# Performance work log

Hardware: AMD Instinct MI355X
Metric: run time of the kernel (lower is better)

## Reference

```python
import jax, jax.numpy as jnp
import numpy as np


def _mlp(h, W_in, b_in, W_hid, b_hid, W_out, b_out):
    # 392 -> 1000 -> (1000)x4 -> 392, ReLU between linear layers (NICE shift net)
    h = jax.nn.relu(h @ W_in + b_in)
    for i in range(W_hid.shape[0]):  # fixed small layer count, not a data dim
        h = jax.nn.relu(h @ W_hid[i] + b_hid[i])
    return h @ W_out + b_out


def setup_inputs() -> dict:
    key = jax.random.key(0)
    ks = jax.random.split(key, 4)
    B, D, MID = 4096, 784, 1000
    half = D // 2
    return {
        "x": jax.random.normal(ks[0], (B, D), jnp.float32),
        "log_det_J": jnp.zeros((1,), jnp.float32),
        "W_in": jax.random.normal(ks[1], (half, MID), jnp.float32) * 0.05,
        "b_in": jnp.zeros((MID,), jnp.float32),
        "W_hid": jax.random.normal(ks[2], (4, MID, MID), jnp.float32) * 0.03,
        "b_hid": jnp.zeros((4, MID), jnp.float32),
        "W_out": jax.random.normal(ks[3], (MID, half), jnp.float32) * 0.03,
        "b_out": jnp.zeros((half,), jnp.float32),
    }


def reference(x, log_det_J, W_in, b_in, W_hid, b_hid, W_out, b_out):
    # mask_config = 0: first = even columns, second = odd columns
    first = x[:, 0::2]   # (B, D/2)
    second = x[:, 1::2]  # (B, D/2)
    shift = _mlp(first, W_in, b_in, W_hid, b_hid, W_out, b_out)
    y_second = second + shift  # coupling_law (reverse=False)
    # interleave: y[:, 0::2] = first, y[:, 1::2] = y_second, in one strided write
    y = jnp.stack([first, y_second], axis=2).reshape(x.shape)
    return (y, log_det_J)
```

## Files before the change

### kernel.cpp

```cpp
#include <hip/hip_runtime.h>

typedef __bf16 bf16;
typedef __bf16 bf16x8 __attribute__((ext_vector_type(8)));
typedef float f32x4 __attribute__((ext_vector_type(4)));

#define M_TOT 4096
#define D_IN  784
#define HALF  392
#define MID   1000
#define K0PAD 448
#define NPAD  1024

__device__ __forceinline__ void g2l16(const bf16* g, bf16* l) {
  __builtin_amdgcn_global_load_lds(
      (__attribute__((address_space(1))) void*)(g),
      (__attribute__((address_space(3))) void*)(l),
      16, 0, 0);
}

__device__ __forceinline__ void wtrans_tile(const float* __restrict__ W, bf16* __restrict__ WT,
                                            int K, int N, int Kpad, int tn, int tk,
                                            float (*tb)[33], int tid) {
  int n0 = tn * 32, k0 = tk * 32;
  int tx = tid & 31, ty = tid >> 5;
#pragma unroll
  for (int r = 0; r < 4; ++r) {
    int k = k0 + ty + 8 * r, n = n0 + tx;
    tb[ty + 8 * r][tx] = (k < K && n < N) ? W[(size_t)k * N + n] : 0.f;
  }
  __syncthreads();
#pragma unroll
  for (int r = 0; r < 4; ++r) {
    int n = n0 + ty + 8 * r, k = k0 + tx;
    WT[(size_t)n * Kpad + k] = (bf16)tb[tx][ty + 8 * r];
  }
}

__global__ void prep_k(const float* __restrict__ x, const float* __restrict__ ldj,
                       const float* __restrict__ W_in,
                       bf16* __restrict__ A0, bf16* __restrict__ WT0,
                       float* __restrict__ y) {
  __shared__ float tb[32][33];
  const int b = blockIdx.x, tid = threadIdx.x;
  if (b < 896) {
    int g = b * 256 + tid;
    int m = g / 56;
    int kq = g - m * 56, k0 = kq * 8;
    bf16x8 v;
    if (k0 < HALF) {
      const float4* xr = (const float4*)(x + (size_t)m * D_IN + 2 * k0);
      float4 a0 = xr[0], a1 = xr[1], a2 = xr[2], a3 = xr[3];
      v[0] = (bf16)a0.x; v[1] = (bf16)a0.z;
      v[2] = (bf16)a1.x; v[3] = (bf16)a1.z;
      v[4] = (bf16)a2.x; v[5] = (bf16)a2.z;
      v[6] = (bf16)a3.x; v[7] = (bf16)a3.z;
    } else {
#pragma unroll
      for (int j = 0; j < 8; ++j) v[j] = (bf16)0.f;
    }
    *(bf16x8*)(A0 + (size_t)m * K0PAD + k0) = v;
    if (b == 0 && tid == 0) y[(size_t)M_TOT * D_IN] = ldj[0];
    return;
  }
  int u = b - 896;
  wtrans_tile(W_in, WT0, HALF, MID, K0PAD, u & 31, u >> 5, tb, tid);
}

template <int BM, int BN, int EPI, int K>
__global__ __launch_bounds__(256, (BM > 64 ? 2 : 4))
void gemm_k(const bf16* __restrict__ A, const bf16* __restrict__ BT,
            const float* __restrict__ bias, int bias_n,
            bf16* __restrict__ C,
            const float* __restrict__ x, float* __restrict__ y, int nb,
            const float* __restrict__ Wx, bf16* __restrict__ WTx,
            int wK, int wN, int wKpad, int wTN) {
  constexpr int BK = 64;
  constexpr int MT = BM / 32, NT = BN / 32;
  constexpr int KT = K / BK;
  constexpr int NBM = M_TOT / BM;
  alignas(16) __shared__ bf16 ldsA[BM * BK];
  alignas(16) __shared__ bf16 ldsB[BN * BK];
  const int tid = threadIdx.x;
  const int id = blockIdx.x;

  if (id >= nb) {
    int u = id - nb;
    wtrans_tile(Wx, WTx, wK, wN, wKpad, u % wTN, u / wTN, (float(*)[33])ldsA, tid);
    return;
  }

  const int wave = tid >> 6, lane = tid & 63;
  const int bm = id % NBM, bn = id / NBM;

  const int srow = lane >> 3;
  const int sq = (lane & 7) ^ srow;
  const bf16* gA = A + ((size_t)bm * BM + wave * (BM / 4) + srow) * K + sq * 8;
  const bf16* gB = BT + ((size_t)bn * BN + wave * (BN / 4) + srow) * K + sq * 8;
  bf16* lA = &ldsA[wave * (BM / 4) * BK];
  bf16* lB = &ldsB[wave * (BN / 4) * BK];

  const int mlane = lane & 15, quad = lane >> 4;
  const int wm = (wave & 1) * (BM / 2), wn = (wave >> 1) * (BN / 2);
  const int axor = mlane & 7;
  const bf16* raBase = &ldsA[(wm + mlane) * BK];
  const bf16* rbBase = &ldsB[(wn + mlane) * BK];

  f32x4 acc[MT][NT] = {};

#pragma unroll
  for (int i = 0; i < BM / 32; ++i) g2l16(gA + (size_t)(8 * i) * K, lA + (8 * i) * BK);
#pragma unroll
  for (int i = 0; i < BN / 32; ++i) g2l16(gB + (size_t)(8 * i) * K, lB + (8 * i) * BK);

  for (int kt = 0; kt < KT; ++kt) {
    __syncthreads();
    bf16x8 af[2][MT], bfr[2][NT];
#pragma unroll
    for (int s = 0; s < 2; ++s) {
      const int co = ((s * 4 + quad) ^ axor) * 8;
#pragma unroll
      for (int i = 0; i < MT; ++i) af[s][i] = *(const bf16x8*)(raBase + i * 16 * BK + co);
#pragma unroll
      for (int i = 0; i < NT; ++i) bfr[s][i] = *(const bf16x8*)(rbBase + i * 16 * BK + co);
    }
    __syncthreads();
    if (kt + 1 < KT) {
      const size_t off = (size_t)(kt + 1) * BK;
#pragma unroll
      for (int i = 0; i < BM / 32; ++i) g2l16(gA + off + (size_t)(8 * i) * K, lA + (8 * i) * BK);
#pragma unroll
      for (int i = 0; i < BN / 32; ++i) g2l16(gB + off + (size_t)(8 * i) * K, lB + (8 * i) * BK);
    }
#pragma unroll
    for (int s = 0; s < 2; ++s)
#pragma unroll
      for (int mt = 0; mt < MT; ++mt)
#pragma unroll
        for (int nt = 0; nt < NT; ++nt)
          acc[mt][nt] = __builtin_amdgcn_mfma_f32_16x16x32_bf16(
              af[s][mt], bfr[s][nt], acc[mt][nt], 0, 0, 0);
  }

  const int ng0 = bn * BN + wn + mlane;
  const int mg0 = bm * BM + wm + quad * 4;

  if (EPI == 0) {
    float bv[NT];
#pragma unroll
    for (int nt = 0; nt < NT; ++nt) {
      int n = ng0 + nt * 16;
      bv[nt] = (n < bias_n) ? bias[n] : 0.f;
    }
#pragma unroll
    for (int mt = 0; mt < MT; ++mt)
#pragma unroll
      for (int nt = 0; nt < NT; ++nt)
#pragma unroll
        for (int r = 0; r < 4; ++r) {
          int m = mg0 + mt * 16 + r;
          int n = ng0 + nt * 16;
          float v = fmaxf(acc[mt][nt][r] + bv[nt], 0.f);
          C[(size_t)m * NPAD + n] = (bf16)v;
        }
  } else {
    const float2* x2 = (const float2*)x;
    float2* y2 = (float2*)y;
#pragma unroll
    for (int nt = 0; nt < NT; ++nt) {
      int n = ng0 + nt * 16;
      if (n < HALF) {
        float bb = bias[n];
#pragma unroll
        for (int mt = 0; mt < MT; ++mt)
#pragma unroll
          for (int r = 0; r < 4; ++r) {
            int m = mg0 + mt * 16 + r;
            size_t off = (size_t)m * (D_IN / 2) + n;
            float2 v = x2[off];
            v.y += acc[mt][nt][r] + bb;
            y2[off] = v;
          }
      }
    }
  }
}

extern "C" void kernel_launch(void* const* d_in, const int* in_sizes, int n_in,
                              void* d_out, int out_size, void* d_ws, size_t ws_size,
                              hipStream_t stream) {
  const float* x     = (const float*)d_in[0];
  const float* ldj   = (const float*)d_in[1];
  const float* W_in  = (const float*)d_in[2];
  const float* b_in  = (const float*)d_in[3];
  const float* W_hid = (const float*)d_in[4];
  const float* b_hid = (const float*)d_in[5];
  const float* W_out = (const float*)d_in[6];
  const float* b_out = (const float*)d_in[7];
  float* y = (float*)d_out;

  char* p = (char*)d_ws;
  bf16* A0  = (bf16*)(p + 0);
  bf16* H0  = (bf16*)(p + 3670016);
  bf16* H1  = (bf16*)(p + 12058624);
  bf16* WT0 = (bf16*)(p + 20447232);
  bf16* WTh = (bf16*)(p + 21364736);
  bf16* WT5 = (bf16*)(p + 29753344);

  const size_t WH = (size_t)NPAD * NPAD;
  const size_t WS = (size_t)MID * MID;

  prep_k<<<dim3(896 + 448), 256, 0, stream>>>(x, ldj, W_in, A0, WT0, y);

  gemm_k<128, 64, 0, K0PAD><<<dim3(512 + 1024), 256, 0, stream>>>(
      A0, WT0, b_in, MID, H0, nullptr, nullptr, 512,
      W_hid + 0 * WS, WTh + 0 * WH, MID, MID, NPAD, 32);
  gemm_k<128, 64, 0, NPAD><<<dim3(512 + 1024), 256, 0, stream>>>(
      H0, WTh + 0 * WH, b_hid + 0 * MID, MID, H1, nullptr, nullptr, 512,
      W_hid + 1 * WS, WTh + 1 * WH, MID, MID, NPAD, 32);
  gemm_k<128, 64, 0, NPAD><<<dim3(512 + 1024), 256, 0, stream>>>(
      H1, WTh + 1 * WH, b_hid + 1 * MID, MID, H0, nullptr, nullptr, 512,
      W_hid + 2 * WS, WTh + 2 * WH, MID, MID, NPAD, 32);
  gemm_k<128, 64, 0, NPAD><<<dim3(512 + 1024), 256, 0, stream>>>(
      H0, WTh + 2 * WH, b_hid + 2 * MID, MID, H1, nullptr, nullptr, 512,
      W_hid + 3 * WS, WTh + 3 * WH, MID, MID, NPAD, 32);
  gemm_k<128, 64, 0, NPAD><<<dim3(512 + 512), 256, 0, stream>>>(
      H1, WTh + 3 * WH, b_hid + 3 * MID, MID, H0, nullptr, nullptr, 512,
      W_out, WT5, MID, HALF, NPAD, 16);
  gemm_k<64, 64, 1, NPAD><<<dim3(512), 256, 0, stream>>>(
      H0, WT5, b_out, HALF, nullptr, x, y, 512,
      nullptr, nullptr, 0, 0, 0, 1);
}
```

Before: 173.4 us.

## Double-buffer LDS tiles with two-stage prefetch and explicit vmcnt waits

Gives the GEMM two LDS buffers for each operand and prefetches two k-tiles ahead. The loop waits with s_waitcnt vmcnt on only the older stage instead of draining every load at a full __syncthreads. This keeps global-to-LDS loads in flight while MFMA runs, to hide memory latency. LDS use doubles, and launch bounds are fixed at 2 waves per EU for all tile sizes, which may lower occupancy for the 64x64 output kernel.

```diff
diff --git a/kernel.cpp b/kernel.cpp
--- a/kernel.cpp
+++ b/kernel.cpp
@@ -67,7 +67,7 @@
 }
 
 template <int BM, int BN, int EPI, int K>
-__global__ __launch_bounds__(256, (BM > 64 ? 2 : 4))
+__global__ __launch_bounds__(256, 2)
 void gemm_k(const bf16* __restrict__ A, const bf16* __restrict__ BT,
             const float* __restrict__ bias, int bias_n,
             bf16* __restrict__ C,
@@ -78,14 +78,18 @@
   constexpr int MT = BM / 32, NT = BN / 32;
   constexpr int KT = K / BK;
   constexpr int NBM = M_TOT / BM;
-  alignas(16) __shared__ bf16 ldsA[BM * BK];
-  alignas(16) __shared__ bf16 ldsB[BN * BK];
+  constexpr int AI = (BM / 4) / 8;
+  constexpr int BI = (BN / 4) / 8;
+  constexpr int LPS = AI + BI;
+  static_assert(K % BK == 0 && KT >= 2, "K/BK");
+  alignas(16) __shared__ bf16 ldsA[2][BM * BK];
+  alignas(16) __shared__ bf16 ldsB[2][BN * BK];
   const int tid = threadIdx.x;
   const int id = blockIdx.x;
 
   if (id >= nb) {
     int u = id - nb;
-    wtrans_tile(Wx, WTx, wK, wN, wKpad, u % wTN, u / wTN, (float(*)[33])ldsA, tid);
+    wtrans_tile(Wx, WTx, wK, wN, wKpad, u % wTN, u / wTN, (float(*)[33])&ldsA[0][0], tid);
     return;
   }
 
@@ -93,44 +97,64 @@
   const int bm = id % NBM, bn = id / NBM;
 
   const int srow = lane >> 3;
-  const int sq = (lane & 7) ^ srow;
-  const bf16* gA = A + ((size_t)bm * BM + wave * (BM / 4) + srow) * K + sq * 8;
-  const bf16* gB = BT + ((size_t)bn * BN + wave * (BN / 4) + srow) * K + sq * 8;
-  bf16* lA = &ldsA[wave * (BM / 4) * BK];
-  bf16* lB = &ldsB[wave * (BN / 4) * BK];
+  const int scol = lane & 7;
+  const bf16* gAb = A + ((size_t)bm * BM + wave * (BM / 4)) * K;
+  const bf16* gBb = BT + ((size_t)bn * BN + wave * (BN / 4)) * K;
+  const int lAo = wave * (BM / 4) * BK;
+  const int lBo = wave * (BN / 4) * BK;
 
   const int mlane = lane & 15, quad = lane >> 4;
   const int wm = (wave & 1) * (BM / 2), wn = (wave >> 1) * (BN / 2);
   const int axor = mlane & 7;
-  const bf16* raBase = &ldsA[(wm + mlane) * BK];
-  const bf16* rbBase = &ldsB[(wn + mlane) * BK];
+
+  auto stage = [&](int kt, int pb) {
+    const int koff = kt * BK;
+#pragma unroll
+    for (int i = 0; i < AI; ++i) {
+      int r = i * 8 + srow;
+      g2l16(gAb + (size_t)r * K + koff + (scol ^ (r & 7)) * 8,
+            &ldsA[pb][lAo + i * 8 * BK]);
+    }
+#pragma unroll
+    for (int i = 0; i < BI; ++i) {
+      int r = i * 8 + srow;
+      g2l16(gBb + (size_t)r * K + koff + (scol ^ (r & 7)) * 8,
+            &ldsB[pb][lBo + i * 8 * BK]);
+    }
+  };
 
   f32x4 acc[MT][NT] = {};
 
-#pragma unroll
-  for (int i = 0; i < BM / 32; ++i) g2l16(gA + (size_t)(8 * i) * K, lA + (8 * i) * BK);
-#pragma unroll
-  for (int i = 0; i < BN / 32; ++i) g2l16(gB + (size_t)(8 * i) * K, lB + (8 * i) * BK);
+  stage(0, 0);
+  stage(1, 1);
 
   for (int kt = 0; kt < KT; ++kt) {
-    __syncthreads();
+    const int pb = kt & 1;
+    if (kt + 1 < KT)
+      asm volatile("s_waitcnt vmcnt(%0)" ::"n"(LPS) : "memory");
+    else
+      asm volatile("s_waitcnt vmcnt(0)" ::: "memory");
+    __builtin_amdgcn_s_barrier();
+    __builtin_amdgcn_sched_barrier(0);
+
+    const bf16* raB = &ldsA[pb][(wm + mlane) * BK];
+    const bf16* rbB = &ldsB[pb][(wn + mlane) * BK];
     bf16x8 af[2][MT], bfr[2][NT];
 #pragma unroll
     for (int s = 0; s < 2; ++s) {
       const int co = ((s * 4 + quad) ^ axor) * 8;
 #pragma unroll
-      for (int i = 0; i < MT; ++i) af[s][i] = *(const bf16x8*)(raBase + i * 16 * BK + co);
-#pragma unroll
-      for (int i = 0; i < NT; ++i) bfr[s][i] = *(const bf16x8*)(rbBase + i * 16 * BK + co);
-    }
-    __syncthreads();
-    if (kt + 1 < KT) {
-      const size_t off = (size_t)(kt + 1) * BK;
-#pragma unroll
-      for (int i = 0; i < BM / 32; ++i) g2l16(gA + off + (size_t)(8 * i) * K, lA + (8 * i) * BK);
-#pragma unroll
-      for (int i = 0; i < BN / 32; ++i) g2l16(gB + off + (size_t)(8 * i) * K, lB + (8 * i) * BK);
-    }
+      for (int i = 0; i < MT; ++i) af[s][i] = *(const bf16x8*)(raB + i * 16 * BK + co);
+#pragma unroll
+      for (int i = 0; i < NT; ++i) bfr[s][i] = *(const bf16x8*)(rbB + i * 16 * BK + co);
+    }
+    asm volatile("s_waitcnt lgkmcnt(0)" ::: "memory");
+    __builtin_amdgcn_sched_barrier(0);
+    __builtin_amdgcn_s_barrier();
+    __builtin_amdgcn_sched_barrier(0);
+
+    if (kt + 2 < KT) stage(kt + 2, pb);
+
 #pragma unroll
     for (int s = 0; s < 2; ++s)
 #pragma unroll
```

Measured after the change: 170.5 us. About the same (-1.7%).
